# Kernel optimization log

Measured on AMD Instinct MI355X. Metric: run time of the kernel, lower is better.

Reference implementation:

```python
import jax, jax.numpy as jnp
import numpy as np

# Repo globals / config
VOCAB_SIZE = 14
TOK_DIM = 8
POS_DIM = 8
D_MODEL = TOK_DIM + POS_DIM  # 16
MAX_SEQ_LEN = 2048
N_HEADS = 2
HEAD_DIM = 3
ATTN_DIM = N_HEADS * HEAD_DIM  # 6
FFN_DIM = 3
B, T = 16, 2048
EPS = 1e-5


def _ln(x, w, b):
    m = jnp.mean(x, axis=-1, keepdims=True)
    v = jnp.var(x, axis=-1, keepdims=True)
    return (x - m) * jax.lax.rsqrt(v + EPS) * w + b


def setup_inputs() -> dict:
    key = jax.random.key(0)
    ks = jax.random.split(key, 20)
    g = lambda k, shape: (jax.random.normal(k, shape, jnp.float32) * 0.1)
    return {
        "idx": jax.random.randint(ks[0], (B, T), 0, VOCAB_SIZE),
        "tok_emb": g(ks[1], (VOCAB_SIZE, TOK_DIM)),
        "pos_enc": g(ks[2], (MAX_SEQ_LEN, POS_DIM)),
        "Wq": g(ks[3], (ATTN_DIM, POS_DIM)),
        "Wk": g(ks[4], (ATTN_DIM, POS_DIM)),
        "Wv": g(ks[5], (ATTN_DIM, TOK_DIM)),
        "Wo": g(ks[6], (D_MODEL, ATTN_DIM)),
        "ln1_w": jnp.ones((D_MODEL,), jnp.float32),
        "ln1_b": jnp.zeros((D_MODEL,), jnp.float32),
        "ln2_w": jnp.ones((D_MODEL,), jnp.float32),
        "ln2_b": jnp.zeros((D_MODEL,), jnp.float32),
        "lnf_w": jnp.ones((D_MODEL,), jnp.float32),
        "lnf_b": jnp.zeros((D_MODEL,), jnp.float32),
        "W1": g(ks[7], (FFN_DIM, D_MODEL)),
        "b1": jnp.zeros((FFN_DIM,), jnp.float32),
        "W2": g(ks[8], (D_MODEL, FFN_DIM)),
        "b2": jnp.zeros((D_MODEL,), jnp.float32),
        "Wh": g(ks[9], (TOK_DIM, D_MODEL)),
    }


def reference(idx, tok_emb, pos_enc, Wq, Wk, Wv, Wo,
              ln1_w, ln1_b, ln2_w, ln2_b, lnf_w, lnf_b,
              W1, b1, W2, b2, Wh):
    Bq, Tq = idx.shape
    tok = tok_emb[idx]                                  # [B,T,TOK_DIM]
    pos = jnp.broadcast_to(pos_enc[:Tq][None], (Bq, Tq, POS_DIM))
    x = jnp.concatenate([tok, pos], axis=-1)            # [B,T,D_MODEL]
    h = _ln(x, ln1_w, ln1_b)
    x_tok = h[..., :TOK_DIM]
    x_pos = h[..., TOK_DIM:]
    # projections (torch Linear: y = x @ W.T)
    q = (x_pos @ Wq.T).reshape(Bq, Tq, N_HEADS, HEAD_DIM).transpose(0, 2, 1, 3)
    k = (x_pos @ Wk.T).reshape(Bq, Tq, N_HEADS, HEAD_DIM).transpose(0, 2, 1, 3)
    v = (x_tok @ Wv.T).reshape(Bq, Tq, N_HEADS, HEAD_DIM).transpose(0, 2, 1, 3)
    scores = jnp.einsum('bhqd,bhkd->bhqk', q, k) / jnp.sqrt(jnp.float32(HEAD_DIM))
    mask = jnp.tril(jnp.ones((Tq, Tq), dtype=bool))
    scores = jnp.where(mask[None, None], scores, -jnp.inf)
    attn = jax.nn.softmax(scores, axis=-1)
    out = jnp.einsum('bhqk,bhkd->bhqd', attn, v)
    out = out.transpose(0, 2, 1, 3).reshape(Bq, Tq, ATTN_DIM)
    x = x + out @ Wo.T
    h2 = _ln(x, ln2_w, ln2_b)
    x = x + (jax.nn.gelu(h2 @ W1.T + b1, approximate=False) @ W2.T + b2)
    x = _ln(x, lnf_w, lnf_b)
    return (x @ Wh.T) @ tok_emb.T                       # tied head -> [B,T,VOCAB]
```

## Files before the change

### kernel.cpp

```cpp
#include <hip/hip_runtime.h>
#include <math.h>

#define BB    16
#define TT    2048
#define VOCAB 14
#define TOKD  8
#define POSD  8
#define DM    16
#define NH    2
#define HD    3
#define AD    6
#define FFND  3

#define NTOK  (BB*TT)
#define BH    (BB*NH)
#define TPB   36
#define NTILE (BH*TPB)

struct P {
    const int*   idx;
    const float* tok_emb;
    const float* pos_enc;
    const float* Wq;
    const float* Wk;
    const float* Wv;
    const float* Wo;
    const float* ln1w;
    const float* ln1b;
    const float* ln2w;
    const float* ln2b;
    const float* lnfw;
    const float* lnfb;
    const float* W1;
    const float* b1;
    const float* W2;
    const float* b2;
    const float* Wh;
    float*       out;
    float4*      pbuf;
};

__device__ __forceinline__ void ln1_of(const P& p, int b, int t, float* h) {
    float x[DM];
    int tok = p.idx[b * TT + t];
    #pragma unroll
    for (int j = 0; j < TOKD; ++j) x[j]        = p.tok_emb[tok * TOKD + j];
    #pragma unroll
    for (int j = 0; j < POSD; ++j) x[TOKD + j] = p.pos_enc[t * POSD + j];

    float m = 0.f;
    #pragma unroll
    for (int j = 0; j < DM; ++j) m += x[j];
    m *= (1.f / DM);
    float v = 0.f;
    #pragma unroll
    for (int j = 0; j < DM; ++j) { float d = x[j] - m; v += d * d; }
    v *= (1.f / DM);
    float rs = rsqrtf(v + 1e-5f);
    #pragma unroll
    for (int j = 0; j < DM; ++j)
        h[j] = (x[j] - m) * rs * p.ln1w[j] + p.ln1b[j];
}

__device__ __forceinline__ float RL(float x, int it) {
    return __uint_as_float(__builtin_amdgcn_readlane(__float_as_uint(x), it));
}

__global__ __launch_bounds__(256) void attn_kernel(P p) {
    __shared__ float4 sq[256];
    __shared__ float4 spart[1024];

    const int tid  = threadIdx.x;
    int tile = blockIdx.x;
    int bh   = tile / TPB;
    int r    = tile - bh * TPB;
    int s    = 0;
    while (((s + 1) * (s + 2)) / 2 <= r) ++s;
    int c    = r - (s * (s + 1)) / 2;
    int b    = bh >> 1;
    int hh   = bh & 1;

    int wv   = tid >> 6;
    int lane = tid & 63;

    float rk0, rk1, rk2, rv0, rv1, rv2;
    {
        float hK[DM];
        ln1_of(p, b, (c << 8) + tid, hK);
        float k0=0.f,k1=0.f,k2=0.f,v0=0.f,v1=0.f,v2=0.f;
        const float* wk  = p.Wk + (hh * 3) * 8;
        const float* wv_ = p.Wv + (hh * 3) * 8;
        #pragma unroll
        for (int j = 0; j < 8; ++j) {
            k0 = fmaf(wk[j],      hK[TOKD + j], k0);
            k1 = fmaf(wk[8 + j],  hK[TOKD + j], k1);
            k2 = fmaf(wk[16 + j], hK[TOKD + j], k2);
            v0 = fmaf(wv_[j],      hK[j], v0);
            v1 = fmaf(wv_[8 + j],  hK[j], v1);
            v2 = fmaf(wv_[16 + j], hK[j], v2);
        }
        rk0 = k0; rk1 = k1; rk2 = k2; rv0 = v0; rv1 = v1; rv2 = v2;

        float hQ[DM];
        if (c != s) {
            ln1_of(p, b, (s << 8) + tid, hQ);
        } else {
            #pragma unroll
            for (int j = 0; j < DM; ++j) hQ[j] = hK[j];
        }
        const float QS = 1.4426950408889634f / 1.7320508075688772f;
        float q0=0.f,q1=0.f,q2=0.f;
        const float* wq = p.Wq + (hh * 3) * 8;
        #pragma unroll
        for (int j = 0; j < 8; ++j) {
            q0 = fmaf(wq[j],      hQ[TOKD + j], q0);
            q1 = fmaf(wq[8 + j],  hQ[TOKD + j], q1);
            q2 = fmaf(wq[16 + j], hQ[TOKD + j], q2);
        }
        sq[tid] = make_float4(q0 * QS, q1 * QS, q2 * QS, 0.f);
    }
    __syncthreads();

    float4 qr[4];
    #pragma unroll
    for (int j = 0; j < 4; ++j) qr[j] = sq[(j << 6) + lane];

    float ac[4][4];
    #pragma unroll
    for (int j = 0; j < 4; ++j)
        ac[j][0] = ac[j][1] = ac[j][2] = ac[j][3] = 0.f;

    if (c < s) {
        #pragma unroll 4
        for (int it = 0; it < 64; ++it) {
            float k0 = RL(rk0, it), k1 = RL(rk1, it), k2 = RL(rk2, it);
            float v0 = RL(rv0, it), v1 = RL(rv1, it), v2 = RL(rv2, it);
            #pragma unroll
            for (int j = 0; j < 4; ++j) {
                float sc = fmaf(qr[j].x, k0, fmaf(qr[j].y, k1, qr[j].z * k2));
                float pr = __builtin_amdgcn_exp2f(sc);
                ac[j][0] = fmaf(pr, v0, ac[j][0]);
                ac[j][1] = fmaf(pr, v1, ac[j][1]);
                ac[j][2] = fmaf(pr, v2, ac[j][2]);
                ac[j][3] += pr;
            }
        }
    } else {
        int kwv = wv << 6;
        #pragma unroll 4
        for (int it = 0; it < 64; ++it) {
            float k0 = RL(rk0, it), k1 = RL(rk1, it), k2 = RL(rk2, it);
            float v0 = RL(rv0, it), v1 = RL(rv1, it), v2 = RL(rv2, it);
            int keyloc = kwv + it;
            #pragma unroll
            for (int j = 0; j < 4; ++j) {
                float sc = fmaf(qr[j].x, k0, fmaf(qr[j].y, k1, qr[j].z * k2));
                float pr = __builtin_amdgcn_exp2f(sc);
                pr = (keyloc <= ((j << 6) + lane)) ? pr : 0.f;
                ac[j][0] = fmaf(pr, v0, ac[j][0]);
                ac[j][1] = fmaf(pr, v1, ac[j][1]);
                ac[j][2] = fmaf(pr, v2, ac[j][2]);
                ac[j][3] += pr;
            }
        }
    }

    #pragma unroll
    for (int j = 0; j < 4; ++j)
        spart[(wv << 8) + (j << 6) + lane] =
            make_float4(ac[j][0], ac[j][1], ac[j][2], ac[j][3]);
    __syncthreads();

    float4 p0 = spart[tid];
    float4 p1 = spart[256 + tid];
    float4 p2 = spart[512 + tid];
    float4 p3 = spart[768 + tid];
    float4 acc = make_float4(p0.x+p1.x+p2.x+p3.x, p0.y+p1.y+p2.y+p3.y,
                             p0.z+p1.z+p2.z+p3.z, p0.w+p1.w+p2.w+p3.w);
    p.pbuf[((size_t)bh * 8 + c) * TT + (s << 8) + tid] = acc;
}

__global__ __launch_bounds__(256) void epi_kernel(P p) {
    int gid = blockIdx.x * 256 + threadIdx.x;
    if (gid >= NTOK) return;
    int t = gid & (TT - 1);
    int b = gid >> 11;
    int s = t >> 8;

    float x[DM];
    int tok = p.idx[gid];
    #pragma unroll
    for (int j = 0; j < TOKD; ++j) x[j]        = p.tok_emb[tok * TOKD + j];
    #pragma unroll
    for (int j = 0; j < POSD; ++j) x[TOKD + j] = p.pos_enc[t * POSD + j];

    float att[AD];
    #pragma unroll
    for (int hh = 0; hh < NH; ++hh) {
        const float4* pp = p.pbuf + ((size_t)(b * NH + hh) * 8) * TT + t;
        float4 acc = pp[0];
        for (int c = 1; c <= s; ++c) {
            float4 e = pp[(size_t)c * TT];
            acc.x += e.x; acc.y += e.y; acc.z += e.z; acc.w += e.w;
        }
        float inv = 1.f / acc.w;
        att[hh*3+0] = acc.x * inv;
        att[hh*3+1] = acc.y * inv;
        att[hh*3+2] = acc.z * inv;
    }

    float xo[DM];
    #pragma unroll
    for (int j = 0; j < DM; ++j) {
        float sacc = x[j];
        #pragma unroll
        for (int a = 0; a < AD; ++a) sacc = fmaf(p.Wo[j * AD + a], att[a], sacc);
        xo[j] = sacc;
    }

    float m = 0.f;
    #pragma unroll
    for (int j = 0; j < DM; ++j) m += xo[j];
    m *= (1.f / DM);
    float v = 0.f;
    #pragma unroll
    for (int j = 0; j < DM; ++j) { float d = xo[j] - m; v += d * d; }
    v *= (1.f / DM);
    float rs = rsqrtf(v + 1e-5f);
    float h2[DM];
    #pragma unroll
    for (int j = 0; j < DM; ++j)
        h2[j] = (xo[j] - m) * rs * p.ln2w[j] + p.ln2b[j];

    float g[FFND];
    #pragma unroll
    for (int cc = 0; cc < FFND; ++cc) {
        float f = p.b1[cc];
        #pragma unroll
        for (int j = 0; j < DM; ++j) f = fmaf(p.W1[cc * DM + j], h2[j], f);
        g[cc] = 0.5f * f * (1.f + erff(f * 0.70710678118654752f));
    }
    float x2[DM];
    #pragma unroll
    for (int j = 0; j < DM; ++j) {
        float sacc = xo[j] + p.b2[j];
        #pragma unroll
        for (int cc = 0; cc < FFND; ++cc) sacc = fmaf(p.W2[j * FFND + cc], g[cc], sacc);
        x2[j] = sacc;
    }

    m = 0.f;
    #pragma unroll
    for (int j = 0; j < DM; ++j) m += x2[j];
    m *= (1.f / DM);
    v = 0.f;
    #pragma unroll
    for (int j = 0; j < DM; ++j) { float d = x2[j] - m; v += d * d; }
    v *= (1.f / DM);
    rs = rsqrtf(v + 1e-5f);
    float y[DM];
    #pragma unroll
    for (int j = 0; j < DM; ++j)
        y[j] = (x2[j] - m) * rs * p.lnfw[j] + p.lnfb[j];

    float t8[TOKD];
    #pragma unroll
    for (int pp = 0; pp < TOKD; ++pp) {
        float sacc = 0.f;
        #pragma unroll
        for (int j = 0; j < DM; ++j) sacc = fmaf(p.Wh[pp * DM + j], y[j], sacc);
        t8[pp] = sacc;
    }
    float* op = p.out + (size_t)gid * VOCAB;
    #pragma unroll
    for (int vcb = 0; vcb < VOCAB; ++vcb) {
        float sacc = 0.f;
        #pragma unroll
        for (int pp = 0; pp < TOKD; ++pp)
            sacc = fmaf(t8[pp], p.tok_emb[vcb * TOKD + pp], sacc);
        op[vcb] = sacc;
    }
}

extern "C" void kernel_launch(void* const* d_in, const int* in_sizes, int n_in,
                              void* d_out, int out_size, void* d_ws, size_t ws_size,
                              hipStream_t stream) {
    P p;
    p.idx     = (const int*)d_in[0];
    p.tok_emb = (const float*)d_in[1];
    p.pos_enc = (const float*)d_in[2];
    p.Wq      = (const float*)d_in[3];
    p.Wk      = (const float*)d_in[4];
    p.Wv      = (const float*)d_in[5];
    p.Wo      = (const float*)d_in[6];
    p.ln1w    = (const float*)d_in[7];
    p.ln1b    = (const float*)d_in[8];
    p.ln2w    = (const float*)d_in[9];
    p.ln2b    = (const float*)d_in[10];
    p.lnfw    = (const float*)d_in[11];
    p.lnfb    = (const float*)d_in[12];
    p.W1      = (const float*)d_in[13];
    p.b1      = (const float*)d_in[14];
    p.W2      = (const float*)d_in[15];
    p.b2      = (const float*)d_in[16];
    p.Wh      = (const float*)d_in[17];
    p.out     = (float*)d_out;
    p.pbuf    = (float4*)d_ws;

    attn_kernel<<<NTILE, 256, 0, stream>>>(p);
    epi_kernel<<<NTOK / 256, 256, 0, stream>>>(p);
}
```

Measured before the change: 131.0 us.

## Use packed FP32 math with LDS-staged K/V and skip masked diagonal subtiles

Replaces readlane broadcasts of K/V with a shared-memory layout that interleaves pairs of keys. This lets the inner loop use packed two-wide FMA (v_pk_fma_f32) on two keys at once. The diagonal tile now skips fully masked query/key wave blocks and applies the mask only on the diagonal sub-block. Launch bounds add an occupancy hint of 5 blocks. The cost is extra LDS traffic for the broadcast loads, plus code duplication in the triangular branch.

Result: faster. 121.7 us (-7.1%).

```diff
diff --git a/kernel.cpp b/kernel.cpp
--- a/kernel.cpp
+++ b/kernel.cpp
@@ -16,6 +16,11 @@
 #define BH    (BB*NH)
 #define TPB   36
 #define NTILE (BH*TPB)
+
+typedef float f2 __attribute__((ext_vector_type(2)));
+__device__ __forceinline__ f2 fma2(f2 a, f2 b, f2 c) {
+    return __builtin_elementwise_fma(a, b, c);
+}
 
 struct P {
     const int*   idx;
@@ -62,11 +67,34 @@
         h[j] = (x[j] - m) * rs * p.ln1w[j] + p.ln1b[j];
 }
 
-__device__ __forceinline__ float RL(float x, int it) {
-    return __uint_as_float(__builtin_amdgcn_readlane(__float_as_uint(x), it));
-}
-
-__global__ __launch_bounds__(256) void attn_kernel(P p) {
+#define PAIR_LOAD(i)                                                           \
+    float4 A  = skv[aw + (i)];                                                 \
+    float4 Bv = skv[128 + aw + (i)];                                           \
+    float4 Cv = skv[256 + aw + (i)];                                           \
+    f2 k0p = {A.x, A.y},  k1p = {A.z, A.w};                                    \
+    f2 k2p = {Bv.x, Bv.y}, v0p = {Bv.z, Bv.w};                                 \
+    f2 v1p = {Cv.x, Cv.y}, v2p = {Cv.z, Cv.w};
+
+#define PAIR_STEP(j)                                                           \
+    { f2 sc = fma2(qx2[j], k0p, fma2(qy2[j], k1p, qz2[j] * k2p));              \
+      f2 pr = {__builtin_amdgcn_exp2f(sc.x), __builtin_amdgcn_exp2f(sc.y)};    \
+      a0[j] = fma2(pr, v0p, a0[j]);                                            \
+      a1[j] = fma2(pr, v1p, a1[j]);                                            \
+      a2[j] = fma2(pr, v2p, a2[j]);                                            \
+      al[j] += pr; }
+
+#define PAIR_STEP_TRI(j, i)                                                    \
+    { f2 sc = fma2(qx2[j], k0p, fma2(qy2[j], k1p, qz2[j] * k2p));              \
+      float pe0 = ((2*(i))   <= lane) ? __builtin_amdgcn_exp2f(sc.x) : 0.f;    \
+      float pe1 = ((2*(i)+1) <= lane) ? __builtin_amdgcn_exp2f(sc.y) : 0.f;    \
+      f2 pr = {pe0, pe1};                                                      \
+      a0[j] = fma2(pr, v0p, a0[j]);                                            \
+      a1[j] = fma2(pr, v1p, a1[j]);                                            \
+      a2[j] = fma2(pr, v2p, a2[j]);                                            \
+      al[j] += pr; }
+
+__global__ __launch_bounds__(256, 5) void attn_kernel(P p) {
+    __shared__ float4 skv[384];
     __shared__ float4 sq[256];
     __shared__ float4 spart[1024];
 
@@ -80,10 +108,6 @@
     int b    = bh >> 1;
     int hh   = bh & 1;
 
-    int wv   = tid >> 6;
-    int lane = tid & 63;
-
-    float rk0, rk1, rk2, rv0, rv1, rv2;
     {
         float hK[DM];
         ln1_of(p, b, (c << 8) + tid, hK);
@@ -99,7 +123,11 @@
             v1 = fmaf(wv_[8 + j],  hK[j], v1);
             v2 = fmaf(wv_[16 + j], hK[j], v2);
         }
-        rk0 = k0; rk1 = k1; rk2 = k2; rv0 = v0; rv1 = v1; rv2 = v2;
+        float* sf = reinterpret_cast<float*>(skv);
+        int o4 = ((tid >> 1) << 2) + (tid & 1);
+        sf[o4]            = k0;  sf[o4 + 2]        = k1;
+        sf[512 + o4]      = k2;  sf[512 + o4 + 2]  = v0;
+        sf[1024 + o4]     = v1;  sf[1024 + o4 + 2] = v2;
 
         float hQ[DM];
         if (c != s) {
@@ -121,46 +149,49 @@
     }
     __syncthreads();
 
-    float4 qr[4];
-    #pragma unroll
-    for (int j = 0; j < 4; ++j) qr[j] = sq[(j << 6) + lane];
-
-    float ac[4][4];
-    #pragma unroll
-    for (int j = 0; j < 4; ++j)
-        ac[j][0] = ac[j][1] = ac[j][2] = ac[j][3] = 0.f;
+    int wv   = tid >> 6;
+    int lane = tid & 63;
+    int aw   = wv << 5;
+
+    f2 qx2[4], qy2[4], qz2[4];
+    #pragma unroll
+    for (int j = 0; j < 4; ++j) {
+        float4 q4 = sq[(j << 6) + lane];
+        qx2[j] = (f2){q4.x, q4.x};
+        qy2[j] = (f2){q4.y, q4.y};
+        qz2[j] = (f2){q4.z, q4.z};
+    }
+
+    f2 a0[4], a1[4], a2[4], al[4];
+    #pragma unroll
+    for (int j = 0; j < 4; ++j) {
+        a0[j] = (f2){0.f, 0.f}; a1[j] = (f2){0.f, 0.f};
+        a2[j] = (f2){0.f, 0.f}; al[j] = (f2){0.f, 0.f};
+    }
 
     if (c < s) {
         #pragma unroll 4
-        for (int it = 0; it < 64; ++it) {
-            float k0 = RL(rk0, it), k1 = RL(rk1, it), k2 = RL(rk2, it);
-            float v0 = RL(rv0, it), v1 = RL(rv1, it), v2 = RL(rv2, it);
+        for (int i = 0; i < 32; ++i) {
+            PAIR_LOAD(i)
             #pragma unroll
-            for (int j = 0; j < 4; ++j) {
-                float sc = fmaf(qr[j].x, k0, fmaf(qr[j].y, k1, qr[j].z * k2));
-                float pr = __builtin_amdgcn_exp2f(sc);
-                ac[j][0] = fmaf(pr, v0, ac[j][0]);
-                ac[j][1] = fmaf(pr, v1, ac[j][1]);
-                ac[j][2] = fmaf(pr, v2, ac[j][2]);
-                ac[j][3] += pr;
-            }
+            for (int j = 0; j < 4; ++j) PAIR_STEP(j)
         }
     } else {
-        int kwv = wv << 6;
-        #pragma unroll 4
-        for (int it = 0; it < 64; ++it) {
-            float k0 = RL(rk0, it), k1 = RL(rk1, it), k2 = RL(rk2, it);
-            float v0 = RL(rv0, it), v1 = RL(rv1, it), v2 = RL(rv2, it);
-            int keyloc = kwv + it;
-            #pragma unroll
-            for (int j = 0; j < 4; ++j) {
-                float sc = fmaf(qr[j].x, k0, fmaf(qr[j].y, k1, qr[j].z * k2));
-                float pr = __builtin_amdgcn_exp2f(sc);
-                pr = (keyloc <= ((j << 6) + lane)) ? pr : 0.f;
-                ac[j][0] = fmaf(pr, v0, ac[j][0]);
-                ac[j][1] = fmaf(pr, v1, ac[j][1]);
-                ac[j][2] = fmaf(pr, v2, ac[j][2]);
-                ac[j][3] += pr;
+        #pragma unroll
+        for (int j = 0; j < 4; ++j) {
+            if (j < wv) continue;
+            if (j == wv) {
+                #pragma unroll 4
+                for (int i = 0; i < 32; ++i) {
+                    PAIR_LOAD(i)
+                    PAIR_STEP_TRI(j, i)
+                }
+            } else {
+                #pragma unroll 4
+                for (int i = 0; i < 32; ++i) {
+                    PAIR_LOAD(i)
+                    PAIR_STEP(j)
+                }
             }
         }
     }
@@ -168,7 +199,8 @@
     #pragma unroll
     for (int j = 0; j < 4; ++j)
         spart[(wv << 8) + (j << 6) + lane] =
-            make_float4(ac[j][0], ac[j][1], ac[j][2], ac[j][3]);
+            make_float4(a0[j].x + a0[j].y, a1[j].x + a1[j].y,
+                        a2[j].x + a2[j].y, al[j].x + al[j].y);
     __syncthreads();
 
     float4 p0 = spart[tid];
```
